# Kernel tuning notes

Hardware: AMD Instinct MI355X
Metric: run time of the kernel (lower is better)

## Reference

```python
import jax, jax.numpy as jnp
import numpy as np

B, S, D = 8, 1024, 1024
H = 16
HD = D // H  # 64


def setup_inputs() -> dict:
    key = jax.random.key(0)
    k1, k2, k3 = jax.random.split(key, 3)
    x = jax.random.normal(k1, (B, S, D), dtype=jnp.float32)
    c_attn_w = jax.random.normal(k2, (D, 3 * D), dtype=jnp.float32) * 0.02
    c_attn_b = jnp.zeros((3 * D,), dtype=jnp.float32)
    c_proj_w = jax.random.normal(k3, (D, D), dtype=jnp.float32) * 0.02
    c_proj_b = jnp.zeros((D,), dtype=jnp.float32)
    return {"x": x, "c_attn_w": c_attn_w, "c_attn_b": c_attn_b,
            "c_proj_w": c_proj_w, "c_proj_b": c_proj_b}


def reference(x, c_attn_w, c_attn_b, c_proj_w, c_proj_b):
    # Conv1D (nx -> 3*nx): x @ W + b
    qkv = x @ c_attn_w + c_attn_b                      # [B,S,3D]
    q, k, v = jnp.split(qkv, 3, axis=-1)               # each [B,S,D]

    def split_heads(t):
        return t.reshape(B, S, H, HD).transpose(0, 2, 1, 3)  # [B,H,S,HD]

    q, k, v = split_heads(q), split_heads(k), split_heads(v)

    # scores, scaled by sqrt(head_dim) since scale=True
    w = jnp.einsum('bhqd,bhkd->bhqk', q, k) / jnp.sqrt(jnp.float32(HD))
    # causal mask exactly as GPT-2 eager: w*b - 10000*(1-b)
    bmask = jnp.tril(jnp.ones((S, S), dtype=w.dtype))[None, None]
    w = w * bmask - 10000.0 * (1.0 - bmask)
    w = jax.nn.softmax(w, axis=-1)
    # attn_dropout p=0.0 -> identity
    a = jnp.einsum('bhqk,bhkd->bhqd', w, v)            # [B,H,S,HD]
    a = a.transpose(0, 2, 1, 3).reshape(B, S, D)       # merge heads
    out = a @ c_proj_w + c_proj_b                      # Conv1D proj
    # resid_dropout p=0.0 -> identity
    return out
```

## Files before the change

### kernel.cpp

```cpp
#include <hip/hip_runtime.h>

#define S_LEN 1024
#define DMODEL 1024
#define NH 16
#define HD 64

typedef unsigned short u16;
typedef __attribute__((ext_vector_type(8))) short short8v;
typedef __attribute__((ext_vector_type(8))) unsigned short ushort8v;
typedef __attribute__((ext_vector_type(4))) float floatx4;

__device__ __forceinline__ u16 f2bf(float f) {
  union { float f; unsigned u; } v; v.f = f;
  unsigned r = v.u + 0x7fffu + ((v.u >> 16) & 1u);
  return (u16)(r >> 16);
}

__device__ __forceinline__ void gld16(const void* g, void* l) {
  __builtin_amdgcn_global_load_lds(
      (const __attribute__((address_space(1))) unsigned int*)g,
      (__attribute__((address_space(3))) unsigned int*)l, 16, 0, 0);
}

__global__ __launch_bounds__(256) void cvt8(const float* __restrict__ in,
                                            u16* __restrict__ out, int n8) {
  int i = blockIdx.x * 256 + threadIdx.x;
  int st = gridDim.x * 256;
  for (; i < n8; i += st) {
    const float4* p = (const float4*)(in + (size_t)i * 8);
    float4 a = p[0], b = p[1];
    ushort8v o;
    o[0] = f2bf(a.x); o[1] = f2bf(a.y); o[2] = f2bf(a.z); o[3] = f2bf(a.w);
    o[4] = f2bf(b.x); o[5] = f2bf(b.y); o[6] = f2bf(b.z); o[7] = f2bf(b.w);
    *(ushort8v*)(out + (size_t)i * 8) = o;
  }
}

__global__ __launch_bounds__(256) void tcvt(const float* __restrict__ in,
                                            u16* __restrict__ out, int R, int C) {
  __shared__ float tile[32][33];
  int c0 = blockIdx.x * 32, r0 = blockIdx.y * 32;
  int tx = threadIdx.x & 31, ty = threadIdx.x >> 5;
#pragma unroll
  for (int i = ty; i < 32; i += 8) tile[i][tx] = in[(size_t)(r0 + i) * C + c0 + tx];
  __syncthreads();
#pragma unroll
  for (int i = ty; i < 32; i += 8)
    out[(size_t)(c0 + i) * R + r0 + tx] = f2bf(tile[tx][i]);
}

template <int OUTBF>
__global__ __launch_bounds__(256) void gemm_bt(const u16* __restrict__ A,
                                               const u16* __restrict__ Bt,
                                               const float* __restrict__ bias,
                                               void* __restrict__ Cout,
                                               int M, int N, int K) {
  __shared__ u16 lA[128 * 64];
  __shared__ u16 lB[128 * 64];
  const int tile_n = blockIdx.x * 128;
  const int tile_m = blockIdx.y * 128;
  const int t = threadIdx.x;
  const int w = t >> 6;
  const int wr = w >> 1, wc = w & 1;
  const int l = t & 63, l16 = l & 15, lq = l >> 4;

  floatx4 acc[4][4] = {};

  const int row_s = t >> 3;
  const int c8 = (t & 7) * 8;
  const int wbase = (t & ~63) * 16;

  for (int kt = 0; kt < K; kt += 64) {
    __syncthreads();
#pragma unroll
    for (int p = 0; p < 4; ++p) {
      int row = p * 32 + row_s;
      gld16(A + (size_t)(tile_m + row) * K + kt + c8, (char*)lA + p * 4096 + wbase);
      gld16(Bt + (size_t)(tile_n + row) * K + kt + c8, (char*)lB + p * 4096 + wbase);
    }
    __syncthreads();
#pragma unroll
    for (int kk = 0; kk < 2; ++kk) {
      short8v af[4], bf[4];
#pragma unroll
      for (int i = 0; i < 4; ++i)
        af[i] = *(const short8v*)&lA[(wr * 64 + i * 16 + l16) * 64 + kk * 32 + lq * 8];
#pragma unroll
      for (int i = 0; i < 4; ++i)
        bf[i] = *(const short8v*)&lB[(wc * 64 + i * 16 + l16) * 64 + kk * 32 + lq * 8];
#pragma unroll
      for (int i = 0; i < 4; ++i)
#pragma unroll
        for (int j = 0; j < 4; ++j)
          acc[i][j] = __builtin_amdgcn_mfma_f32_16x16x32_bf16(af[i], bf[j], acc[i][j], 0, 0, 0);
    }
  }
#pragma unroll
  for (int i = 0; i < 4; ++i) {
#pragma unroll
    for (int j = 0; j < 4; ++j) {
      int col = tile_n + wc * 64 + j * 16 + l16;
      float bv = bias[col];
#pragma unroll
      for (int r = 0; r < 4; ++r) {
        int row = tile_m + wr * 64 + i * 16 + lq * 4 + r;
        float v = acc[i][j][r] + bv;
        if (OUTBF)
          ((u16*)Cout)[(size_t)row * N + col] = f2bf(v);
        else
          ((float*)Cout)[(size_t)row * N + col] = v;
      }
    }
  }
}

__global__ __launch_bounds__(256) void vtrans(const u16* __restrict__ qkv,
                                              u16* __restrict__ vt) {
  __shared__ u16 tile[64][68];
  int bh = blockIdx.y, b = bh >> 4, h = bh & 15;
  int s0 = blockIdx.x * 64;
  int t = threadIdx.x;
  for (int i = t; i < 512; i += 256) {
    int s = i >> 3, c0 = (i & 7) * 8;
    ushort8v v = *(const ushort8v*)(qkv + (size_t)(b * S_LEN + s0 + s) * 3072 +
                                    2 * DMODEL + h * HD + c0);
#pragma unroll
    for (int j = 0; j < 8; ++j) tile[s][c0 + j] = v[j];
  }
  __syncthreads();
  for (int i = t; i < 512; i += 256) {
    int hd = i >> 3, s1 = (i & 7) * 8;
    ushort8v v;
#pragma unroll
    for (int j = 0; j < 8; ++j) v[j] = tile[s1 + j][hd];
    *(ushort8v*)(vt + (size_t)bh * (HD * S_LEN) + (size_t)hd * S_LEN + s0 + s1) = v;
  }
}

__global__ __launch_bounds__(256) void attn_fwd2(const u16* __restrict__ qkv,
                                                 const u16* __restrict__ vt,
                                                 u16* __restrict__ aout) {
  __shared__ u16 lK[64 * 64];
  __shared__ u16 lV[64 * 64];
  __shared__ u16 pl[4][16 * 72];
  const int bh = blockIdx.x, qx = blockIdx.y;
  const int b = bh >> 4, h = bh & 15;
  const int t = threadIdx.x, w = t >> 6, l = t & 63;
  const int l16 = l & 15, lq = l >> 4;

  const int srow = t >> 3;
  const int sslot = (t & 7) ^ (srow & 7);
  const u16* kS = qkv + (size_t)(b * S_LEN + srow) * 3072 + DMODEL + h * HD + sslot * 8;
  const u16* vS = vt + (size_t)bh * (HD * S_LEN) + (size_t)srow * S_LEN + sslot * 8;
  char* ldK = (char*)lK + (t & ~63) * 16;
  char* ldV = (char*)lV + (t & ~63) * 16;

  u16* myp = &pl[w][0];
  const int cswz = (l16 & 7) << 3;

#pragma unroll 1
  for (int half = 0; half < 2; ++half) {
    const int qb = half ? (15 - qx) : qx;
    const int qrow0 = qb * 64 + w * 16;

    const u16* qptr = qkv + (size_t)(b * S_LEN + qrow0 + l16) * 3072 + h * HD;
    short8v qf0 = *(const short8v*)(qptr + lq * 8);
    short8v qf1 = *(const short8v*)(qptr + 32 + lq * 8);

    floatx4 accO[4] = {};
    float mrow[4] = {-1e30f, -1e30f, -1e30f, -1e30f};
    float lrow[4] = {0.f, 0.f, 0.f, 0.f};

#pragma unroll 1
    for (int kb = 0; kb <= qb; ++kb) {
      const int kv0 = kb * 64;
      __syncthreads();
      gld16(kS + (size_t)kv0 * 3072, ldK);
      gld16(kS + (size_t)(kv0 + 32) * 3072, ldK + 4096);
      gld16(vS + kv0, ldV);
      gld16(vS + kv0 + (size_t)32 * S_LEN, ldV + 4096);
      __syncthreads();

      floatx4 sc[4];
#pragma unroll
      for (int sg = 0; sg < 4; ++sg) {
        const int rowb = (sg * 16 + l16) * 64;
        short8v kA = *(const short8v*)&lK[rowb + ((lq * 8) ^ cswz)];
        short8v kB = *(const short8v*)&lK[rowb + ((32 + lq * 8) ^ cswz)];
        floatx4 sa = {};
        sa = __builtin_amdgcn_mfma_f32_16x16x32_bf16(qf0, kA, sa, 0, 0, 0);
        sa = __builtin_amdgcn_mfma_f32_16x16x32_bf16(qf1, kB, sa, 0, 0, 0);
        sc[sg] = sa;
      }

      const bool diag = (kb == qb);
      float scl[4];
#pragma unroll
      for (int r = 0; r < 4; ++r) {
        const int srw = qrow0 + lq * 4 + r;
        float v[4];
#pragma unroll
        for (int sg = 0; sg < 4; ++sg) {
          v[sg] = sc[sg][r] * 0.125f;
          if (diag) {
            const int scol = kv0 + sg * 16 + l16;
            if (scol > srw) v[sg] = -10000.0f;
          }
        }
        float mx = fmaxf(fmaxf(v[0], v[1]), fmaxf(v[2], v[3]));
        mx = fmaxf(mx, __shfl_xor(mx, 1));
        mx = fmaxf(mx, __shfl_xor(mx, 2));
        mx = fmaxf(mx, __shfl_xor(mx, 4));
        mx = fmaxf(mx, __shfl_xor(mx, 8));
        const float mnew = fmaxf(mrow[r], mx);
        const float sres = __expf(mrow[r] - mnew);
        mrow[r] = mnew;
        float ps = 0.f;
        float p[4];
#pragma unroll
        for (int sg = 0; sg < 4; ++sg) {
          p[sg] = __expf(v[sg] - mnew);
          ps += p[sg];
        }
        ps += __shfl_xor(ps, 1);
        ps += __shfl_xor(ps, 2);
        ps += __shfl_xor(ps, 4);
        ps += __shfl_xor(ps, 8);
        lrow[r] = lrow[r] * sres + ps;
        scl[r] = sres;
#pragma unroll
        for (int sg = 0; sg < 4; ++sg)
          myp[(lq * 4 + r) * 72 + sg * 16 + l16] = f2bf(p[sg]);
      }
#pragma unroll
      for (int n = 0; n < 4; ++n)
#pragma unroll
        for (int r = 0; r < 4; ++r) accO[n][r] *= scl[r];

      short8v pf0 = *(const short8v*)&myp[l16 * 72 + lq * 8];
      short8v pf1 = *(const short8v*)&myp[l16 * 72 + 32 + lq * 8];
#pragma unroll
      for (int n = 0; n < 4; ++n) {
        const int rowb = (n * 16 + l16) * 64;
        short8v v0 = *(const short8v*)&lV[rowb + ((lq * 8) ^ cswz)];
        short8v v1 = *(const short8v*)&lV[rowb + ((32 + lq * 8) ^ cswz)];
        accO[n] = __builtin_amdgcn_mfma_f32_16x16x32_bf16(pf0, v0, accO[n], 0, 0, 0);
        accO[n] = __builtin_amdgcn_mfma_f32_16x16x32_bf16(pf1, v1, accO[n], 0, 0, 0);
      }
    }

#pragma unroll
    for (int n = 0; n < 4; ++n)
#pragma unroll
      for (int r = 0; r < 4; ++r) {
        const int srw = qrow0 + lq * 4 + r;
        aout[(size_t)(b * S_LEN + srw) * DMODEL + h * HD + n * 16 + l16] =
            f2bf(accO[n][r] / lrow[r]);
      }
  }
}

extern "C" void kernel_launch(void* const* d_in, const int* in_sizes, int n_in,
                              void* d_out, int out_size, void* d_ws, size_t ws_size,
                              hipStream_t stream) {
  const float* x = (const float*)d_in[0];
  const float* w1 = (const float*)d_in[1];
  const float* b1 = (const float*)d_in[2];
  const float* w2 = (const float*)d_in[3];
  const float* b2 = (const float*)d_in[4];
  float* out = (float*)d_out;
  char* ws = (char*)d_ws;

  u16* xb = (u16*)(ws + 0);
  u16* w1t = (u16*)(ws + 16777216);
  u16* w2t = (u16*)(ws + 23068672);
  u16* qkvb = (u16*)(ws + 25165824);
  u16* vtb = (u16*)(ws + 75497472);
  u16* ab = (u16*)(ws + 92274688);
  if (ws_size < 109051904) return;

  hipLaunchKernelGGL(cvt8, dim3(2048), dim3(256), 0, stream, x, xb, 1048576);
  hipLaunchKernelGGL(tcvt, dim3(96, 32), dim3(256), 0, stream, w1, w1t, 1024, 3072);
  hipLaunchKernelGGL(tcvt, dim3(32, 32), dim3(256), 0, stream, w2, w2t, 1024, 1024);
  hipLaunchKernelGGL((gemm_bt<1>), dim3(24, 64), dim3(256), 0, stream,
                     xb, w1t, b1, (void*)qkvb, 8192, 3072, 1024);
  hipLaunchKernelGGL(vtrans, dim3(16, 128), dim3(256), 0, stream, qkvb, vtb);
  hipLaunchKernelGGL(attn_fwd2, dim3(128, 8), dim3(256), 0, stream, qkvb, vtb, ab);
  hipLaunchKernelGGL((gemm_bt<0>), dim3(8, 64), dim3(256), 0, stream,
                     ab, w2t, b2, (void*)out, 8192, 1024, 1024);
}
```

Baseline: 280.8 us.

## Replace GEMM with triple-buffered 128x256-tile kernel using swizzled LDS

Replaces the 128x128 single-buffered bf16 GEMM with a 512-thread kernel that computes 128x256 tiles. It uses three LDS stages filled asynchronously by global_load_lds, with explicit vmcnt waits and one barrier per k-step, so global loads overlap the MFMA work. An XOR swizzle on LDS columns is meant to avoid bank conflicts. A workgroup index remap groups tiles across XCDs, and s_setprio raises priority around the MFMA blocks. The 144KB of dynamic LDS allows only one block per CU, and the larger tiles mean fewer workgroups for the 1024-wide projection GEMM.

```diff
diff --git a/kernel.cpp b/kernel.cpp
--- a/kernel.cpp
+++ b/kernel.cpp
@@ -50,61 +50,103 @@
 }
 
 template <int OUTBF>
-__global__ __launch_bounds__(256) void gemm_bt(const u16* __restrict__ A,
-                                               const u16* __restrict__ Bt,
-                                               const float* __restrict__ bias,
-                                               void* __restrict__ Cout,
-                                               int M, int N, int K) {
-  __shared__ u16 lA[128 * 64];
-  __shared__ u16 lB[128 * 64];
-  const int tile_n = blockIdx.x * 128;
-  const int tile_m = blockIdx.y * 128;
+__global__ __launch_bounds__(512, 2) void gemm3(const u16* __restrict__ A,
+                                                const u16* __restrict__ Bt,
+                                                const float* __restrict__ bias,
+                                                void* __restrict__ Cout,
+                                                int M, int N, int K) {
+  extern __shared__ u16 lds[];
+  const int nbx = N >> 8;
+  const int nwg = nbx * (M >> 7);
+  const int orig = blockIdx.x;
+  const int cpx = nwg >> 3;
+  const int swz = (orig & 7) * cpx + (orig >> 3);
+  const int tile_n = (swz % nbx) << 8;
+  const int tile_m = (swz / nbx) << 7;
+
   const int t = threadIdx.x;
-  const int w = t >> 6;
-  const int wr = w >> 1, wc = w & 1;
-  const int l = t & 63, l16 = l & 15, lq = l >> 4;
+  const int w = t >> 6, l = t & 63;
+  const int wm = w >> 2, wn = w & 3;
+  const int l16 = l & 15, lq = l >> 4;
+  const int cswz = (l16 & 7) << 3;
+
+  const int srow = t >> 3;
+  const int sslot = (t & 7) ^ (srow & 7);
+  const u16* aS = A + (size_t)(tile_m + srow) * K + sslot * 8;
+  const u16* bS = Bt + (size_t)(tile_n + srow) * K + sslot * 8;
+  char* ldsc = (char*)lds;
+  const int dst16 = t * 16;
 
   floatx4 acc[4][4] = {};
-
-  const int row_s = t >> 3;
-  const int c8 = (t & 7) * 8;
-  const int wbase = (t & ~63) * 16;
-
-  for (int kt = 0; kt < K; kt += 64) {
-    __syncthreads();
-#pragma unroll
-    for (int p = 0; p < 4; ++p) {
-      int row = p * 32 + row_s;
-      gld16(A + (size_t)(tile_m + row) * K + kt + c8, (char*)lA + p * 4096 + wbase);
-      gld16(Bt + (size_t)(tile_n + row) * K + kt + c8, (char*)lB + p * 4096 + wbase);
+  const int NT = K >> 6;
+
+#pragma unroll
+  for (int pt = 0; pt < 2; ++pt) {
+    char* bb = ldsc + pt * 49152;
+    const int kt = pt << 6;
+#pragma unroll
+    for (int j = 0; j < 2; ++j)
+      gld16(aS + (size_t)(j * 64) * K + kt, bb + j * 8192 + dst16);
+#pragma unroll
+    for (int j = 0; j < 4; ++j)
+      gld16(bS + (size_t)(j * 64) * K + kt, bb + 16384 + j * 8192 + dst16);
+  }
+
+  int cur = 0, nxt2 = 2;
+  for (int tt = 0; tt < NT; ++tt) {
+    if (tt + 1 < NT) asm volatile("s_waitcnt vmcnt(6)" ::: "memory");
+    else             asm volatile("s_waitcnt vmcnt(0)" ::: "memory");
+    __builtin_amdgcn_sched_barrier(0);
+    __builtin_amdgcn_s_barrier();
+    __builtin_amdgcn_sched_barrier(0);
+
+    if (tt + 2 < NT) {
+      char* bb = ldsc + nxt2 * 49152;
+      const int kt = (tt + 2) << 6;
+#pragma unroll
+      for (int j = 0; j < 2; ++j)
+        gld16(aS + (size_t)(j * 64) * K + kt, bb + j * 8192 + dst16);
+#pragma unroll
+      for (int j = 0; j < 4; ++j)
+        gld16(bS + (size_t)(j * 64) * K + kt, bb + 16384 + j * 8192 + dst16);
     }
-    __syncthreads();
+
+    const u16* bA = lds + cur * 24576;
+    const u16* bB = bA + 8192;
 #pragma unroll
     for (int kk = 0; kk < 2; ++kk) {
       short8v af[4], bf[4];
 #pragma unroll
       for (int i = 0; i < 4; ++i)
-        af[i] = *(const short8v*)&lA[(wr * 64 + i * 16 + l16) * 64 + kk * 32 + lq * 8];
+        af[i] = *(const short8v*)&bA[(wm * 64 + i * 16 + l16) * 64 +
+                                     ((kk * 32 + lq * 8) ^ cswz)];
+#pragma unroll
+      for (int j = 0; j < 4; ++j)
+        bf[j] = *(const short8v*)&bB[(wn * 64 + j * 16 + l16) * 64 +
+                                     ((kk * 32 + lq * 8) ^ cswz)];
+      __builtin_amdgcn_s_setprio(1);
 #pragma unroll
       for (int i = 0; i < 4; ++i)
-        bf[i] = *(const short8v*)&lB[(wc * 64 + i * 16 + l16) * 64 + kk * 32 + lq * 8];
-#pragma unroll
-      for (int i = 0; i < 4; ++i)
 #pragma unroll
         for (int j = 0; j < 4; ++j)
-          acc[i][j] = __builtin_amdgcn_mfma_f32_16x16x32_bf16(af[i], bf[j], acc[i][j], 0, 0, 0);
+          acc[i][j] = __builtin_amdgcn_mfma_f32_16x16x32_bf16(af[i], bf[j],
+                                                              acc[i][j], 0, 0, 0);
+      __builtin_amdgcn_s_setprio(0);
     }
-  }
+    cur = (cur == 2) ? 0 : cur + 1;
+    nxt2 = (nxt2 == 2) ? 0 : nxt2 + 1;
+  }
+
 #pragma unroll
   for (int i = 0; i < 4; ++i) {
 #pragma unroll
     for (int j = 0; j < 4; ++j) {
-      int col = tile_n + wc * 64 + j * 16 + l16;
-      float bv = bias[col];
+      const int col = tile_n + wn * 64 + j * 16 + l16;
+      const float bv = bias[col];
 #pragma unroll
       for (int r = 0; r < 4; ++r) {
-        int row = tile_m + wr * 64 + i * 16 + lq * 4 + r;
-        float v = acc[i][j][r] + bv;
+        const int row = tile_m + wm * 64 + i * 16 + lq * 4 + r;
+        const float v = acc[i][j][r] + bv;
         if (OUTBF)
           ((u16*)Cout)[(size_t)row * N + col] = f2bf(v);
         else
@@ -279,13 +321,18 @@
   u16* ab = (u16*)(ws + 92274688);
   if (ws_size < 109051904) return;
 
+  hipFuncSetAttribute(reinterpret_cast<const void*>(gemm3<1>),
+                      hipFuncAttributeMaxDynamicSharedMemorySize, 147456);
+  hipFuncSetAttribute(reinterpret_cast<const void*>(gemm3<0>),
+                      hipFuncAttributeMaxDynamicSharedMemorySize, 147456);
+
   hipLaunchKernelGGL(cvt8, dim3(2048), dim3(256), 0, stream, x, xb, 1048576);
   hipLaunchKernelGGL(tcvt, dim3(96, 32), dim3(256), 0, stream, w1, w1t, 1024, 3072);
   hipLaunchKernelGGL(tcvt, dim3(32, 32), dim3(256), 0, stream, w2, w2t, 1024, 1024);
-  hipLaunchKernelGGL((gemm_bt<1>), dim3(24, 64), dim3(256), 0, stream,
+  hipLaunchKernelGGL((gemm3<1>), dim3(768), dim3(512), 147456, stream,
                      xb, w1t, b1, (void*)qkvb, 8192, 3072, 1024);
   hipLaunchKernelGGL(vtrans, dim3(16, 128), dim3(256), 0, stream, qkvb, vtb);
   hipLaunchKernelGGL(attn_fwd2, dim3(128, 8), dim3(256), 0, stream, qkvb, vtb, ab);
-  hipLaunchKernelGGL((gemm_bt<0>), dim3(8, 64), dim3(256), 0, stream,
+  hipLaunchKernelGGL((gemm3<0>), dim3(256), dim3(512), 147456, stream,
                      ab, w2t, b2, (void*)out, 8192, 1024, 1024);
 }
```

Result: faster. 271.1 us (-3.5%).
